# Performance work log

Hardware: AMD Instinct MI355X
Metric: run time of the kernel (lower is better)

The kernel has to match this reference:

```python
import jax, jax.numpy as jnp
import numpy as np

N_NODES = 50000
IN_CH = 128
HIDDEN = 256
N_EDGES = 800000


def setup_inputs() -> dict:
    key = jax.random.key(0)
    k_z, k_e, k_w1, k_b1, k_w2, k_b2 = jax.random.split(key, 6)
    z = jax.random.normal(k_z, (N_NODES, IN_CH), dtype=jnp.float32)
    edge_index = jax.random.randint(k_e, (2, N_EDGES), 0, N_NODES, dtype=jnp.int64)
    # nn.Linear params (stored as [in, out] for x @ W + b)
    lim1 = 1.0 / np.sqrt(2 * IN_CH)
    W1 = jax.random.uniform(k_w1, (2 * IN_CH, HIDDEN), minval=-lim1, maxval=lim1, dtype=jnp.float32)
    b1 = jax.random.uniform(k_b1, (HIDDEN,), minval=-lim1, maxval=lim1, dtype=jnp.float32)
    lim2 = 1.0 / np.sqrt(HIDDEN)
    W2 = jax.random.uniform(k_w2, (HIDDEN, 1), minval=-lim2, maxval=lim2, dtype=jnp.float32)
    b2 = jax.random.uniform(k_b2, (1,), minval=-lim2, maxval=lim2, dtype=jnp.float32)
    return {"z": z, "edge_index": edge_index, "W1": W1, "b1": b1, "W2": W2, "b2": b2}


def reference(z, edge_index, W1, b1, W2, b2):
    row, col = edge_index[0], edge_index[1]
    # gather endpoint embeddings and concat -> [E, 2*in_ch]
    edge_features = jnp.concatenate([z[row], z[col]], axis=1)
    h = jax.nn.relu(edge_features @ W1 + b1)   # [E, hidden]
    logits = (h @ W2 + b2).squeeze(-1)         # [E]
    return jax.nn.sigmoid(logits)
```

## Files before the change

### kernel.cpp

```cpp
#include <hip/hip_runtime.h>
#include <hip/hip_bf16.h>
#include <cstdint>
#include <cstddef>

#define N_EDGES_C 800000
#define N_NODES_C 50000
#define IN_CH_C   128
#define KDIM      256
#define HIDDEN_C  256

typedef __attribute__((ext_vector_type(8))) short sh8;
typedef __attribute__((ext_vector_type(4))) float f32x4;

__device__ __forceinline__ unsigned short f2bf(float f) {
  union { float f; unsigned u; } a; a.f = f;
  unsigned r = a.u + 0x7fffu + ((a.u >> 16) & 1u);
  return (unsigned short)(r >> 16);
}

__device__ __forceinline__ void glds16(const unsigned short* g, void* l) {
  __builtin_amdgcn_global_load_lds(
      (const __attribute__((address_space(1))) unsigned int*)g,
      (__attribute__((address_space(3))) unsigned int*)l, 16, 0, 0);
}


__global__ void cvt_w1ct_kernel(const float* __restrict__ w1,
                                unsigned short* __restrict__ w1ct) {
  const int k = blockIdx.x;
  const int j = threadIdx.x;
  const float v = (j < 256) ? w1[(size_t)k * 256 + j]
                            : w1[(size_t)(128 + k) * 256 + (j - 256)];
  w1ct[(size_t)j * 128 + k] = f2bf(v);
}

__global__ __launch_bounds__(512) void build_zw_kernel(
    const float* __restrict__ z,
    const unsigned short* __restrict__ w1ct,
    const float* __restrict__ b1,
    unsigned short* __restrict__ zw)
{
  __shared__ __align__(16) unsigned char Az[16384];
  const int tid = threadIdx.x;
  const int w   = tid >> 6;
  const int l   = tid & 63;
  const int l15 = l & 15;
  const int lg  = l >> 4;
  const int nb  = blockIdx.x;
  const int j0  = w * 64;

  {
    const int row = tid >> 3;
    const int fc  = (tid & 7) * 16;
    int node = nb * 64 + row;
    node = (node < N_NODES_C) ? node : (N_NODES_C - 1);
    const float4* zp = reinterpret_cast<const float4*>(
        z + (size_t)node * IN_CH_C + fc);
    float4 x0 = zp[0], x1 = zp[1], x2 = zp[2], x3 = zp[3];
    sh8 o0, o1;
    o0[0]=(short)f2bf(x0.x); o0[1]=(short)f2bf(x0.y); o0[2]=(short)f2bf(x0.z); o0[3]=(short)f2bf(x0.w);
    o0[4]=(short)f2bf(x1.x); o0[5]=(short)f2bf(x1.y); o0[6]=(short)f2bf(x1.z); o0[7]=(short)f2bf(x1.w);
    o1[0]=(short)f2bf(x2.x); o1[1]=(short)f2bf(x2.y); o1[2]=(short)f2bf(x2.z); o1[3]=(short)f2bf(x2.w);
    o1[4]=(short)f2bf(x3.x); o1[5]=(short)f2bf(x3.y); o1[6]=(short)f2bf(x3.z); o1[7]=(short)f2bf(x3.w);
    const int c0  = fc * 2;
    const int swz = (row & 7) << 4;
    *reinterpret_cast<sh8*>(Az + row * 256 + (c0 ^ swz))        = o0;
    *reinterpret_cast<sh8*>(Az + row * 256 + ((c0 + 16) ^ swz)) = o1;
  }

  sh8 bfr[4][4];
#pragma unroll
  for (int nt = 0; nt < 4; ++nt)
#pragma unroll
    for (int kk = 0; kk < 4; ++kk)
      bfr[nt][kk] = *reinterpret_cast<const sh8*>(
          w1ct + (size_t)(j0 + nt * 16 + l15) * 128 + kk * 32 + lg * 8);

  __syncthreads();

  const f32x4 fz = {0.f, 0.f, 0.f, 0.f};
  f32x4 acc[4][4];
#pragma unroll
  for (int mt = 0; mt < 4; ++mt)
#pragma unroll
    for (int nt = 0; nt < 4; ++nt)
      acc[mt][nt] = fz;

#pragma unroll
  for (int kk = 0; kk < 4; ++kk) {
#pragma unroll
    for (int mt = 0; mt < 4; ++mt) {
      const int row = mt * 16 + l15;
      const sh8 af = *reinterpret_cast<const sh8*>(
          Az + row * 256 + ((kk * 64 + lg * 16) ^ ((l15 & 7) << 4)));
#pragma unroll
      for (int nt = 0; nt < 4; ++nt)
        acc[mt][nt] = __builtin_amdgcn_mfma_f32_16x16x32_bf16(
            af, bfr[nt][kk], acc[mt][nt], 0, 0, 0);
    }
  }

#pragma unroll
  for (int nt = 0; nt < 4; ++nt) {
    const int j = j0 + nt * 16 + l15;
    const float bb = (j < 256) ? b1[j] : 0.f;
#pragma unroll
    for (int mt = 0; mt < 4; ++mt) {
#pragma unroll
      for (int r = 0; r < 4; ++r) {
        const int node = nb * 64 + mt * 16 + lg * 4 + r;
        if (node < N_NODES_C)
          zw[(size_t)node * 512 + j] = f2bf(acc[mt][nt][r] + bb);
      }
    }
  }
}

#define UNPACK2(u, v, wa, wb)                                              \
  {                                                                        \
    float lo_ = __uint_as_float((u) << 16) + __uint_as_float((v) << 16);   \
    float hi_ = __uint_as_float((u) & 0xffff0000u) +                       \
                __uint_as_float((v) & 0xffff0000u);                        \
    a0 = fmaf(fmaxf(lo_, 0.f), (wa), a0);                                  \
    a1 = fmaf(fmaxf(hi_, 0.f), (wb), a1);                                  \
  }
#define STEP4(T, B, Wa, Wb)                                                \
  UNPACK2((T).x, (B).x, (Wa).x, (Wa).y)                                    \
  UNPACK2((T).y, (B).y, (Wa).z, (Wa).w)                                    \
  UNPACK2((T).z, (B).z, (Wb).x, (Wb).y)                                    \
  UNPACK2((T).w, (B).w, (Wb).z, (Wb).w)

__global__ __launch_bounds__(256) void edge_pass_kernel(
    const unsigned short* __restrict__ zw,
    const int* __restrict__ ei,
    const float* __restrict__ w2,
    const float* __restrict__ b2,
    float* __restrict__ out)
{
  const int tid = threadIdx.x;
  const int w   = tid >> 6;
  const int l   = tid & 63;
  const int g   = l >> 3;
  const int q   = l & 7;
  const int e   = blockIdx.x * 32 + w * 8 + g;

  const int r = ei[e];
  const int c = ei[N_EDGES_C + e];

  const uint4* tp = reinterpret_cast<const uint4*>(zw + (size_t)r * 512 + q * 32);
  const uint4* bp = reinterpret_cast<const uint4*>(zw + (size_t)c * 512 + 256 + q * 32);
  const float4* wp = reinterpret_cast<const float4*>(w2 + q * 32);

  uint4 T0 = tp[0], T1 = tp[1], T2 = tp[2], T3 = tp[3];
  uint4 B0 = bp[0], B1 = bp[1], B2 = bp[2], B3 = bp[3];
  float4 W0 = wp[0], W1 = wp[1], W2c = wp[2], W3 = wp[3];
  float4 W4 = wp[4], W5 = wp[5], W6 = wp[6], W7 = wp[7];
  const float b2v = b2[0];
  __builtin_amdgcn_sched_barrier(0);

  float a0 = 0.f, a1 = 0.f;
  STEP4(T0, B0, W0, W1)
  STEP4(T1, B1, W2c, W3)
  STEP4(T2, B2, W4, W5)
  STEP4(T3, B3, W6, W7)

  float s = a0 + a1;
  s += __shfl_xor(s, 1, 64);
  s += __shfl_xor(s, 2, 64);
  s += __shfl_xor(s, 4, 64);
  if (q == 0)
    out[e] = 1.f / (1.f + __expf(-(s + b2v)));
}

#define TM        32
#define NBLK      512
#define THREADS   512

__global__ void cvt_z_kernel(const float* __restrict__ z,
                             unsigned short* __restrict__ zb) {
  int i = blockIdx.x * blockDim.x + threadIdx.x;
  float4 v = reinterpret_cast<const float4*>(z)[i];
  ushort4 o;
  o.x = f2bf(v.x); o.y = f2bf(v.y); o.z = f2bf(v.z); o.w = f2bf(v.w);
  reinterpret_cast<ushort4*>(zb)[i] = o;
}

__global__ void cvt_w1t_kernel(const float* __restrict__ w1,
                               unsigned short* __restrict__ w1t) {
  int k = blockIdx.x;
  int n = threadIdx.x;
  w1t[(size_t)n * KDIM + k] = f2bf(w1[(size_t)k * HIDDEN_C + n]);
}

__global__ __launch_bounds__(THREADS, 4) void decoder_persist(
    const unsigned short* __restrict__ zb,
    const int* __restrict__ ei,
    const unsigned short* __restrict__ w1t,
    const float* __restrict__ b1,
    const float* __restrict__ w2,
    const float* __restrict__ b2,
    float* __restrict__ out)
{
  __shared__ __align__(16) unsigned char lds[3 * 16384 + 2048];
  float* red = (float*)(lds + 3 * 16384);

  const int tid = threadIdx.x;
  const int w   = tid >> 6;
  const int l   = tid & 63;
  const int l15 = l & 15;
  const int lg  = l >> 4;
  const int n0  = w * 32;

  const int b    = blockIdx.x;
  const bool big = (b < 424);
  const int ntb  = big ? 49 : 48;
  const int S    = big ? (49 * b) : (49 * 424 + 48 * (b - 424));
  const int tb   = S * TM;

  const int nd   = (l >> 4) & 1;
  const int eo0  = 4 * w + (l >> 5);
  const int eo1  = eo0 + 2;
  const int sc   = (l & 31) * 16;
  const int off0 = (sc ^ ((eo0 & 7) << 4)) & 255;
  const int off1 = (sc ^ ((eo1 & 7) << 4)) & 255;
  const int* eip0 = ei + (size_t)nd * N_EDGES_C + tb + eo0;
  const int* eip1 = ei + (size_t)nd * N_EDGES_C + tb + eo1;

  sh8 bfr[2][8];
#pragma unroll
  for (int nt = 0; nt < 2; ++nt)
#pragma unroll
    for (int kk = 0; kk < 8; ++kk)
      bfr[nt][kk] = *reinterpret_cast<const sh8*>(
          w1t + (size_t)(n0 + nt * 16 + l15) * KDIM + kk * 32 + lg * 8);

  const float b1v0 = b1[n0 + l15],      b1v1 = b1[n0 + 16 + l15];
  const float w2v0 = w2[n0 + l15],      w2v1 = w2[n0 + 16 + l15];
  const float b2v  = b2[0];

  const int b2b = (l15 >> 2) & 1;
  const int Eb  = l15 * 512 + 64 * b2b + ((lg * 16) ^ ((l15 & 3) << 4));
  const int Ob  = Eb - 128 * b2b;

  int ia0 = eip0[0],      ia1 = eip1[0];
  __builtin_amdgcn_sched_barrier(0);
  int ib0 = eip0[TM],     ib1 = eip1[TM];
  __builtin_amdgcn_sched_barrier(0);
  glds16(zb + (size_t)ia0 * IN_CH_C + (off0 >> 1), lds + 0 * 16384 + (2 * w + 0) * 1024);
  glds16(zb + (size_t)ia1 * IN_CH_C + (off1 >> 1), lds + 0 * 16384 + (2 * w + 1) * 1024);
  __builtin_amdgcn_sched_barrier(0);
  int jc0 = eip0[2 * TM], jc1 = eip1[2 * TM];
  __builtin_amdgcn_sched_barrier(0);
  glds16(zb + (size_t)ib0 * IN_CH_C + (off0 >> 1), lds + 1 * 16384 + (2 * w + 0) * 1024);
  glds16(zb + (size_t)ib1 * IN_CH_C + (off1 >> 1), lds + 1 * 16384 + (2 * w + 1) * 1024);
  __builtin_amdgcn_sched_barrier(0);

  int cur = 0, nx1 = 16384, nx2 = 32768;

#pragma unroll 1
  for (int t = 0; t < ntb; ++t) {
    __builtin_amdgcn_sched_barrier(0);
    asm volatile("s_waitcnt vmcnt(4) lgkmcnt(0)" ::: "memory");
    __builtin_amdgcn_s_barrier();
    __builtin_amdgcn_sched_barrier(0);

    const int tn = (t + 3 < ntb) ? (t + 3) : (ntb - 1);
    int ni0 = eip0[tn * TM];
    int ni1 = eip1[tn * TM];
    __builtin_amdgcn_sched_barrier(0);

    glds16(zb + (size_t)jc0 * IN_CH_C + (off0 >> 1), lds + nx2 + (2 * w + 0) * 1024);
    glds16(zb + (size_t)jc1 * IN_CH_C + (off1 >> 1), lds + nx2 + (2 * w + 1) * 1024);
    __builtin_amdgcn_sched_barrier(0);

    const f32x4 fz = {0.f, 0.f, 0.f, 0.f};
    f32x4 acc[2][2] = {{fz, fz}, {fz, fz}};
    __builtin_amdgcn_s_setprio(1);
#pragma unroll
    for (int kk = 0; kk < 8; ++kk) {
      const int kb_ = ((kk & 1) ? Ob : Eb) + kk * 64;
#pragma unroll
      for (int mt = 0; mt < 2; ++mt) {
        const sh8 af = *reinterpret_cast<const sh8*>(lds + cur + kb_ + mt * 8192);
        acc[mt][0] = __builtin_amdgcn_mfma_f32_16x16x32_bf16(af, bfr[0][kk], acc[mt][0], 0, 0, 0);
        acc[mt][1] = __builtin_amdgcn_mfma_f32_16x16x32_bf16(af, bfr[1][kk], acc[mt][1], 0, 0, 0);
      }
    }
    __builtin_amdgcn_s_setprio(0);

    float pl[2][4];
#pragma unroll
    for (int mt = 0; mt < 2; ++mt)
#pragma unroll
      for (int r = 0; r < 4; ++r) {
        float v0 = fmaxf(acc[mt][0][r] + b1v0, 0.f);
        float v1 = fmaxf(acc[mt][1][r] + b1v1, 0.f);
        pl[mt][r] = v0 * w2v0 + v1 * w2v1;
      }
#pragma unroll
    for (int s = 1; s < 16; s <<= 1)
#pragma unroll
      for (int mt = 0; mt < 2; ++mt)
#pragma unroll
        for (int r = 0; r < 4; ++r)
          pl[mt][r] += __shfl_xor(pl[mt][r], s, 64);
    if (l15 == 0) {
#pragma unroll
      for (int mt = 0; mt < 2; ++mt) {
        float4 v = make_float4(pl[mt][0], pl[mt][1], pl[mt][2], pl[mt][3]);
        *reinterpret_cast<float4*>(&red[(t & 1) * 256 + w * 32 + mt * 16 + lg * 4]) = v;
      }
    }

    if (t > 0 && tid < TM) {
      float s = b2v;
#pragma unroll
      for (int ww = 0; ww < 8; ++ww)
        s += red[((t - 1) & 1) * 256 + ww * 32 + tid];
      out[tb + (t - 1) * TM + tid] = 1.f / (1.f + __expf(-s));
    }

    jc0 = ni0; jc1 = ni1;
    int tmp = cur; cur = nx1; nx1 = nx2; nx2 = tmp;
  }

  __builtin_amdgcn_sched_barrier(0);
  asm volatile("s_waitcnt lgkmcnt(0)" ::: "memory");
  __builtin_amdgcn_s_barrier();
  __builtin_amdgcn_sched_barrier(0);
  if (tid < TM) {
    float s = b2v;
#pragma unroll
    for (int ww = 0; ww < 8; ++ww)
      s += red[((ntb - 1) & 1) * 256 + ww * 32 + tid];
    out[tb + (ntb - 1) * TM + tid] = 1.f / (1.f + __expf(-s));
  }
  asm volatile("s_waitcnt vmcnt(0)" ::: "memory");
}

#define BM 64
__global__ __launch_bounds__(512, 6) void decoder_fb(
    const float* __restrict__ z, const int* __restrict__ ei,
    const unsigned short* __restrict__ w1t, const float* __restrict__ b1,
    const float* __restrict__ w2, const float* __restrict__ b2,
    float* __restrict__ out)
{
  __shared__ __align__(16) unsigned char lds[BM * 512];
  const int tid = threadIdx.x, wave = tid >> 6, lane = tid & 63;
  const int l15 = lane & 15, lg = lane >> 4, base = blockIdx.x * BM;
  {
    const int e = tid & 63, w8 = tid >> 6, nd = w8 >> 2;
    const int idx = ei[nd * N_EDGES_C + base + e];
    const int swzw = (e & 7) << 4;
    char* dstrow = (char*)lds + e * 512;
    const float* src = z + (size_t)idx * IN_CH_C + (w8 & 3) * 32;
    float4 tf[8];
#pragma unroll
    for (int i = 0; i < 8; ++i) tf[i] = reinterpret_cast<const float4*>(src)[i];
#pragma unroll
    for (int i = 0; i < 4; ++i) {
      sh8 o; const float4 x0 = tf[2*i], x1 = tf[2*i+1];
      o[0]=(short)f2bf(x0.x); o[1]=(short)f2bf(x0.y); o[2]=(short)f2bf(x0.z); o[3]=(short)f2bf(x0.w);
      o[4]=(short)f2bf(x1.x); o[5]=(short)f2bf(x1.y); o[6]=(short)f2bf(x1.z); o[7]=(short)f2bf(x1.w);
      *reinterpret_cast<sh8*>(dstrow + ((w8 * 64 + i * 16) ^ swzw)) = o;
    }
  }
  __syncthreads();
  const int n0 = wave * 32;
  const int swz = (l15 & 7) << 4;
  const int Ebase = l15 * 512 + ((lg * 16) ^ swz);
  const int Obase = Ebase - ((swz & 64) << 1);
  const f32x4 fz = {0.f,0.f,0.f,0.f};
  f32x4 acc[4][2];
#pragma unroll
  for (int mt = 0; mt < 4; ++mt) { acc[mt][0] = fz; acc[mt][1] = fz; }
#pragma unroll
  for (int kk = 0; kk < 8; ++kk) {
    const int kOff = kk * 32 + lg * 8;
    sh8 bfrag[2];
#pragma unroll
    for (int nt = 0; nt < 2; ++nt)
      bfrag[nt] = *reinterpret_cast<const sh8*>(w1t + (size_t)(n0 + nt*16 + l15) * KDIM + kOff);
    const int kbase = ((kk & 1) ? Obase : Ebase) + kk * 64;
#pragma unroll
    for (int mt = 0; mt < 4; ++mt) {
      const sh8 af = *reinterpret_cast<const sh8*>((char*)lds + (kbase + mt * 8192));
      acc[mt][0] = __builtin_amdgcn_mfma_f32_16x16x32_bf16(af, bfrag[0], acc[mt][0], 0, 0, 0);
      acc[mt][1] = __builtin_amdgcn_mfma_f32_16x16x32_bf16(af, bfrag[1], acc[mt][1], 0, 0, 0);
    }
  }
  float plog[4][4];
#pragma unroll
  for (int mt = 0; mt < 4; ++mt)
#pragma unroll
    for (int r = 0; r < 4; ++r) plog[mt][r] = 0.f;
#pragma unroll
  for (int nt = 0; nt < 2; ++nt) {
    const int j = n0 + nt * 16 + l15;
    const float b1v = b1[j], w2v = w2[j];
#pragma unroll
    for (int mt = 0; mt < 4; ++mt)
#pragma unroll
      for (int r = 0; r < 4; ++r)
        plog[mt][r] = fmaf(fmaxf(acc[mt][nt][r] + b1v, 0.f), w2v, plog[mt][r]);
  }
#pragma unroll
  for (int s = 1; s < 16; s <<= 1)
#pragma unroll
    for (int mt = 0; mt < 4; ++mt)
#pragma unroll
      for (int r = 0; r < 4; ++r)
        plog[mt][r] += __shfl_xor(plog[mt][r], s, 64);
  __syncthreads();
  float* red = (float*)lds;
  if (l15 == 0)
#pragma unroll
    for (int mt = 0; mt < 4; ++mt)
#pragma unroll
      for (int r = 0; r < 4; ++r)
        red[wave * 64 + mt * 16 + lg * 4 + r] = plog[mt][r];
  __syncthreads();
  if (tid < BM) {
    float s = b2[0];
#pragma unroll
    for (int w = 0; w < 8; ++w) s += red[w * 64 + tid];
    out[base + tid] = 1.f / (1.f + __expf(-s));
  }
}

extern "C" void kernel_launch(void* const* d_in, const int* in_sizes, int n_in,
                              void* d_out, int out_size, void* d_ws, size_t ws_size,
                              hipStream_t stream) {
  const float* z  = (const float*)d_in[0];
  const int*   ei = (const int*)d_in[1];
  const float* W1 = (const float*)d_in[2];
  const float* b1 = (const float*)d_in[3];
  const float* W2 = (const float*)d_in[4];
  const float* b2 = (const float*)d_in[5];
  float* out = (float*)d_out;

  const size_t o_w1   = 0;
  const size_t o_zw   = 131072;
  const size_t need_A = o_zw + (size_t)N_NODES_C * 512 * 2;
  const size_t need_mid = 131072 + (size_t)N_NODES_C * IN_CH_C * 2;

  if (ws_size >= need_A) {
    unsigned short* w1ct = (unsigned short*)((char*)d_ws + o_w1);
    unsigned short* zw   = (unsigned short*)((char*)d_ws + o_zw);
    cvt_w1ct_kernel<<<128, 512, 0, stream>>>(W1, w1ct);
    build_zw_kernel<<<(N_NODES_C + 63) / 64, 512, 0, stream>>>(z, w1ct, b1, zw);
    edge_pass_kernel<<<N_EDGES_C / 32, 256, 0, stream>>>(zw, ei, W2, b2, out);
  } else if (ws_size >= need_mid) {
    unsigned short* w1t = (unsigned short*)d_ws;
    unsigned short* zb  = (unsigned short*)((char*)d_ws + 131072);
    cvt_w1t_kernel<<<KDIM, HIDDEN_C, 0, stream>>>(W1, w1t);
    cvt_z_kernel<<<(N_NODES_C * IN_CH_C / 4) / 256, 256, 0, stream>>>(z, zb);
    decoder_persist<<<NBLK, THREADS, 0, stream>>>(zb, ei, w1t, b1, W2, b2, out);
  } else {
    unsigned short* w1t = (unsigned short*)d_ws;
    cvt_w1t_kernel<<<KDIM, HIDDEN_C, 0, stream>>>(W1, w1t);
    decoder_fb<<<N_EDGES_C / BM, 512, 0, stream>>>(z, ei, w1t, b1, W2, b2, out);
  }
}
```

Before: 185.7 us.

## Software-pipeline edge gathers with inline-asm loads, eight edges per 16-lane group

The edge pass now gives each 16-lane group eight consecutive edges instead of one edge per 8-lane group. Row and column gathers and the index loads are issued ahead with inline-asm global loads in a two-stage double buffer, paced by manual vmcnt waits. The aim is to hide gather latency and amortise the W2 loads and launch overhead over more edges per thread. The cost is fragile hand-counted waitcnts that depend on how the compiler emits the other loads, plus fewer blocks, which lowers the parallelism available to hide latency.

Result: faster. 160.6 us (-13.5%).

```diff
diff --git a/kernel.cpp b/kernel.cpp
--- a/kernel.cpp
+++ b/kernel.cpp
@@ -116,6 +116,13 @@
   }
 }
 
+#define GLDX4_0(dst, p)  asm volatile("global_load_dwordx4 %0, %1, off"            : "=v"(dst) : "v"(p))
+#define GLDX4_16(dst, p) asm volatile("global_load_dwordx4 %0, %1, off offset:16"  : "=v"(dst) : "v"(p))
+#define GLDW(dst, p)     asm volatile("global_load_dword %0, %1, off"              : "=v"(dst) : "v"(p))
+#define VMWAIT(N)                                                          \
+  asm volatile("s_waitcnt vmcnt(" #N ")" ::: "memory");                    \
+  __builtin_amdgcn_sched_barrier(0);
+
 #define UNPACK2(u, v, wa, wb)                                              \
   {                                                                        \
     float lo_ = __uint_as_float((u) << 16) + __uint_as_float((v) << 16);   \
@@ -130,7 +137,7 @@
   UNPACK2((T).z, (B).z, (Wb).x, (Wb).y)                                    \
   UNPACK2((T).w, (B).w, (Wb).z, (Wb).w)
 
-__global__ __launch_bounds__(256) void edge_pass_kernel(
+__global__ __launch_bounds__(256, 5) void edge_pass_pipe(
     const unsigned short* __restrict__ zw,
     const int* __restrict__ ei,
     const float* __restrict__ w2,
@@ -138,38 +145,70 @@
     float* __restrict__ out)
 {
   const int tid = threadIdx.x;
-  const int w   = tid >> 6;
-  const int l   = tid & 63;
-  const int g   = l >> 3;
-  const int q   = l & 7;
-  const int e   = blockIdx.x * 32 + w * 8 + g;
-
-  const int r = ei[e];
-  const int c = ei[N_EDGES_C + e];
-
-  const uint4* tp = reinterpret_cast<const uint4*>(zw + (size_t)r * 512 + q * 32);
-  const uint4* bp = reinterpret_cast<const uint4*>(zw + (size_t)c * 512 + 256 + q * 32);
-  const float4* wp = reinterpret_cast<const float4*>(w2 + q * 32);
-
-  uint4 T0 = tp[0], T1 = tp[1], T2 = tp[2], T3 = tp[3];
-  uint4 B0 = bp[0], B1 = bp[1], B2 = bp[2], B3 = bp[3];
-  float4 W0 = wp[0], W1 = wp[1], W2c = wp[2], W3 = wp[3];
-  float4 W4 = wp[4], W5 = wp[5], W6 = wp[6], W7 = wp[7];
+  const int q   = tid & 15;
+  const int G   = (blockIdx.x * 256 + tid) >> 4;
+  const int e0  = G * 8;
+
+  const float4* wp = reinterpret_cast<const float4*>(w2 + q * 16);
+  const float4 W0 = wp[0], W1 = wp[1], W2r = wp[2], W3 = wp[3];
   const float b2v = b2[0];
-  __builtin_amdgcn_sched_barrier(0);
-
-  float a0 = 0.f, a1 = 0.f;
-  STEP4(T0, B0, W0, W1)
-  STEP4(T1, B1, W2c, W3)
-  STEP4(T2, B2, W4, W5)
-  STEP4(T3, B3, W6, W7)
-
-  float s = a0 + a1;
-  s += __shfl_xor(s, 1, 64);
-  s += __shfl_xor(s, 2, 64);
-  s += __shfl_xor(s, 4, 64);
-  if (q == 0)
-    out[e] = 1.f / (1.f + __expf(-(s + b2v)));
+
+  const char* zwB = (const char*)zw;
+  const int   qo  = q * 32;
+
+  int rr[10], cc[10];
+  rr[8] = 0; cc[8] = 0; rr[9] = 0; cc[9] = 0;
+  rr[0] = ei[e0];     cc[0] = ei[N_EDGES_C + e0];
+  rr[1] = ei[e0 + 1]; cc[1] = ei[N_EDGES_C + e0 + 1];
+
+  uint4 Tf[2][2], Bf[2][2];
+  {
+    const char* ta = zwB + ((size_t)(unsigned)rr[0] << 10) + qo;
+    const char* tb = zwB + ((size_t)(unsigned)cc[0] << 10) + 512 + qo;
+    GLDX4_0(Tf[0][0], ta); GLDX4_16(Tf[0][1], ta);
+    GLDX4_0(Bf[0][0], tb); GLDX4_16(Bf[0][1], tb);
+  }
+  GLDW(rr[2], (const void*)(ei + e0 + 2));
+  GLDW(cc[2], (const void*)(ei + N_EDGES_C + e0 + 2));
+  {
+    const char* ta = zwB + ((size_t)(unsigned)rr[1] << 10) + qo;
+    const char* tb = zwB + ((size_t)(unsigned)cc[1] << 10) + 512 + qo;
+    GLDX4_0(Tf[1][0], ta); GLDX4_16(Tf[1][1], ta);
+    GLDX4_0(Bf[1][0], tb); GLDX4_16(Bf[1][1], tb);
+  }
+  GLDW(rr[3], (const void*)(ei + e0 + 3));
+  GLDW(cc[3], (const void*)(ei + N_EDGES_C + e0 + 3));
+
+#pragma unroll
+  for (int i = 0; i < 8; ++i) {
+    const int s = i & 1;
+    if (i <= 4)      { VMWAIT(6) }
+    else if (i <= 6) { VMWAIT(4) }
+    else             { VMWAIT(0) }
+
+    float a0 = 0.f, a1 = 0.f;
+    STEP4(Tf[s][0], Bf[s][0], W0, W1)
+    STEP4(Tf[s][1], Bf[s][1], W2r, W3)
+    float v = a0 + a1;
+    v += __shfl_xor(v, 1, 64);
+    v += __shfl_xor(v, 2, 64);
+    v += __shfl_xor(v, 4, 64);
+    v += __shfl_xor(v, 8, 64);
+    if (q == 0)
+      out[e0 + i] = 1.f / (1.f + __expf(-(v + b2v)));
+
+    if (i <= 5) {
+      const char* ta = zwB + ((size_t)(unsigned)rr[i + 2] << 10) + qo;
+      const char* tb = zwB + ((size_t)(unsigned)cc[i + 2] << 10) + 512 + qo;
+      GLDX4_0(Tf[s][0], ta); GLDX4_16(Tf[s][1], ta);
+      GLDX4_0(Bf[s][0], tb); GLDX4_16(Bf[s][1], tb);
+    }
+    if (i <= 3) {
+      GLDW(rr[i + 4], (const void*)(ei + e0 + i + 4));
+      GLDW(cc[i + 4], (const void*)(ei + N_EDGES_C + e0 + i + 4));
+    }
+  }
+  asm volatile("s_waitcnt vmcnt(0)" ::: "memory");
 }
 
 #define TM        32
@@ -449,7 +488,7 @@
     unsigned short* zw   = (unsigned short*)((char*)d_ws + o_zw);
     cvt_w1ct_kernel<<<128, 512, 0, stream>>>(W1, w1ct);
     build_zw_kernel<<<(N_NODES_C + 63) / 64, 512, 0, stream>>>(z, w1ct, b1, zw);
-    edge_pass_kernel<<<N_EDGES_C / 32, 256, 0, stream>>>(zw, ei, W2, b2, out);
+    edge_pass_pipe<<<N_EDGES_C / 128, 256, 0, stream>>>(zw, ei, W2, b2, out);
   } else if (ws_size >= need_mid) {
     unsigned short* w1t = (unsigned short*)d_ws;
     unsigned short* zb  = (unsigned short*)((char*)d_ws + 131072);
```
